# Kernel tuning notes

Measured on AMD Instinct MI355X. Metric: run time of the kernel, lower is better.

Reference implementation:

```python
import jax, jax.numpy as jnp
import numpy as np
from jax import lax

K = 3  # local kernel size (k in the module)
PAD = K // 2

def _conv2d(x, w, b, pad):
    # x: [B,Cin,H,W], w: [Cout,Cin,kh,kw]
    y = lax.conv_general_dilated(
        x, w, window_strides=(1, 1), padding=[(pad, pad), (pad, pad)],
        dimension_numbers=('NCHW', 'OIHW', 'NCHW'))
    return y + b[None, :, None, None]

def setup_inputs() -> dict:
    key = jax.random.key(0)
    ks = jax.random.split(key, 4)
    B, C, H, W = 8, 64, 256, 256
    lr_t = jax.random.normal(ks[0], (B, 3, H, W), dtype=jnp.float32)
    h_tm1 = jax.random.normal(ks[1], (B, C, H, W), dtype=jnp.float32)
    w1 = jax.random.normal(ks[2], (C, 3, 3, 3), dtype=jnp.float32) * (1.0 / np.sqrt(3 * 9))
    b1 = jnp.zeros((C,), dtype=jnp.float32)
    w2 = jax.random.normal(ks[3], (K * K, C, 1, 1), dtype=jnp.float32) * (1.0 / np.sqrt(C))
    b2 = jnp.zeros((K * K,), dtype=jnp.float32)
    return {"lr_t": lr_t, "h_tm1": h_tm1, "w1": w1, "b1": b1, "w2": w2, "b2": b2}

def reference(lr_t, h_tm1, w1, b1, w2, b2):
    B, C, H, W = h_tm1.shape
    # k_proj: Conv2d(3,dim,3,p=1) -> ReLU -> Conv2d(dim,k^2,1)
    kern = _conv2d(jax.nn.relu(_conv2d(lr_t, w1, b1, 1)), w2, b2, 0)  # [B,k^2,H,W]
    # Fused unfold * kernel -> sum over k^2 taps, without materializing [B,C,H,W,k^2].
    # F.unfold orders taps row-major: tap index = i*K + j.
    h_pad = jnp.pad(h_tm1, ((0, 0), (0, 0), (PAD, PAD), (PAD, PAD)))
    sim = jnp.zeros_like(h_tm1)
    for i in range(K):
        for j in range(K):
            shifted = lax.dynamic_slice(h_pad, (0, 0, i, j), (B, C, H, W))
            sim = sim + shifted * kern[:, i * K + j][:, None, :, :]
    return h_tm1 * jax.nn.sigmoid(sim)
```

## Files before the change

kernel.cpp:

```cpp
#include <hip/hip_runtime.h>
#include <hip/hip_bf16.h>
#include <math.h>

constexpr int B_  = 8;
constexpr int CIN = 3;
constexpr int C_  = 64;
constexpr int H_  = 256;
constexpr int W_  = 256;
constexpr int TAPS = 9;

typedef float f32x4 __attribute__((ext_vector_type(4)));

__global__ __launch_bounds__(256, 4)
void hsa_kern(const float* __restrict__ lr,
              const float* __restrict__ w1,
              const float* __restrict__ b1,
              const float* __restrict__ w2,
              const float* __restrict__ b2,
              float* __restrict__ kws)
{
    __shared__ float w2t[C_][12];

    const int tid = threadIdx.x;
    const int blk = blockIdx.x;
    const int b = blk / H_;
    const int y = blk % H_;

    for (int i = tid; i < TAPS * C_; i += 256) {
        const int t = i / C_;
        const int c = i % C_;
        w2t[c][t] = w2[i];
    }
    __syncthreads();

    const int x = tid;
    float win[CIN][3][3];
    #pragma unroll
    for (int ci = 0; ci < CIN; ++ci) {
        #pragma unroll
        for (int r = 0; r < 3; ++r) {
            const int yy = y + r - 1;
            const bool vy = (unsigned)yy < (unsigned)H_;
            const float* row = lr + ((size_t)(b * CIN + ci) * H_ + yy) * W_;
            win[ci][r][0] = (vy && x > 0)       ? row[x - 1] : 0.f;
            win[ci][r][1] = vy                   ? row[x]     : 0.f;
            win[ci][r][2] = (vy && x < W_ - 1)  ? row[x + 1] : 0.f;
        }
    }

    float acc[TAPS];
    #pragma unroll
    for (int t = 0; t < TAPS; ++t) acc[t] = b2[t];

    for (int c = 0; c < C_; ++c) {
        const float* wc = w1 + c * 27;
        float h0 = b1[c], h1 = 0.f, h2 = 0.f;
        #pragma unroll
        for (int r = 0; r < 3; ++r)
            #pragma unroll
            for (int j = 0; j < 3; ++j) {
                h0 = fmaf(wc[(0 * 3 + r) * 3 + j], win[0][r][j], h0);
                h1 = fmaf(wc[(1 * 3 + r) * 3 + j], win[1][r][j], h1);
                h2 = fmaf(wc[(2 * 3 + r) * 3 + j], win[2][r][j], h2);
            }
        const float hsum = fmaxf((h0 + h1) + h2, 0.f);

        const float4 wa = *(const float4*)&w2t[c][0];
        const float4 wb = *(const float4*)&w2t[c][4];
        const float  w8 = w2t[c][8];
        acc[0] = fmaf(wa.x, hsum, acc[0]);
        acc[1] = fmaf(wa.y, hsum, acc[1]);
        acc[2] = fmaf(wa.z, hsum, acc[2]);
        acc[3] = fmaf(wa.w, hsum, acc[3]);
        acc[4] = fmaf(wb.x, hsum, acc[4]);
        acc[5] = fmaf(wb.y, hsum, acc[5]);
        acc[6] = fmaf(wb.z, hsum, acc[6]);
        acc[7] = fmaf(wb.w, hsum, acc[7]);
        acc[8] = fmaf(w8,  hsum, acc[8]);
    }

    float* kr = kws + (size_t)(b * H_ + y) * TAPS * W_;
    #pragma unroll
    for (int t = 0; t < TAPS; ++t) kr[t * W_ + x] = acc[t];
}

__global__ __launch_bounds__(256, 8)
void hsa_gate(const float* __restrict__ hin,
              const float* __restrict__ kws,
              float* __restrict__ out)
{
    __shared__ float kernS[TAPS][W_];

    const int tid = threadIdx.x;
    const int bid = blockIdx.x;
    const int nb  = (bid & 7) * (B_ * H_ / 8) + (bid >> 3);
    const int b = nb / H_;
    const int y = nb % H_;

    const float* kr = kws + (size_t)(b * H_ + y) * TAPS * W_;
    for (int i = tid; i < TAPS * W_; i += 256)
        ((float*)kernS)[i] = kr[i];
    __syncthreads();

    const int lane = tid & 63;
    const int wav  = tid >> 6;
    const int x0   = lane * 4;

    float4 kt[TAPS];
    #pragma unroll
    for (int t = 0; t < TAPS; ++t) kt[t] = *(const float4*)&kernS[t][x0];

    #pragma unroll 4
    for (int cc = 0; cc < 16; ++cc) {
        const int c = wav * 16 + cc;
        const float* hb = hin + (size_t)(b * C_ + c) * H_ * W_;

        float4 rowv[3];
        float  lft[3], rgt[3];
        #pragma unroll
        for (int r = 0; r < 3; ++r) {
            const int yy = y + r - 1;
            const bool vy = (unsigned)yy < (unsigned)H_;
            float4 m;
            if (vy) m = *(const float4*)(hb + (size_t)yy * W_ + x0);
            else    m = make_float4(0.f, 0.f, 0.f, 0.f);
            rowv[r] = m;
            float l  = __shfl_up(m.w, 1);
            float rr = __shfl_down(m.x, 1);
            if (lane == 0)  l  = 0.f;
            if (lane == 63) rr = 0.f;
            lft[r] = l; rgt[r] = rr;
        }

        float sim0 = 0.f, sim1 = 0.f, sim2 = 0.f, sim3 = 0.f;
        #pragma unroll
        for (int r = 0; r < 3; ++r) {
            const float w6_0 = lft[r];
            const float w6_1 = rowv[r].x;
            const float w6_2 = rowv[r].y;
            const float w6_3 = rowv[r].z;
            const float w6_4 = rowv[r].w;
            const float w6_5 = rgt[r];
            {
                const float4 k4 = kt[r * 3 + 0];
                sim0 = fmaf(w6_0, k4.x, sim0);
                sim1 = fmaf(w6_1, k4.y, sim1);
                sim2 = fmaf(w6_2, k4.z, sim2);
                sim3 = fmaf(w6_3, k4.w, sim3);
            }
            {
                const float4 k4 = kt[r * 3 + 1];
                sim0 = fmaf(w6_1, k4.x, sim0);
                sim1 = fmaf(w6_2, k4.y, sim1);
                sim2 = fmaf(w6_3, k4.z, sim2);
                sim3 = fmaf(w6_4, k4.w, sim3);
            }
            {
                const float4 k4 = kt[r * 3 + 2];
                sim0 = fmaf(w6_2, k4.x, sim0);
                sim1 = fmaf(w6_3, k4.y, sim1);
                sim2 = fmaf(w6_4, k4.z, sim2);
                sim3 = fmaf(w6_5, k4.w, sim3);
            }
        }

        f32x4 o;
        o.x = rowv[1].x * __builtin_amdgcn_rcpf(1.f + __expf(-sim0));
        o.y = rowv[1].y * __builtin_amdgcn_rcpf(1.f + __expf(-sim1));
        o.z = rowv[1].z * __builtin_amdgcn_rcpf(1.f + __expf(-sim2));
        o.w = rowv[1].w * __builtin_amdgcn_rcpf(1.f + __expf(-sim3));
        __builtin_nontemporal_store(o, (f32x4*)(out + ((size_t)(b * C_ + c) * H_ + y) * W_ + x0));
    }
}

__global__ __launch_bounds__(256, 4)
void hsa_fused(const float* __restrict__ lr,
               const float* __restrict__ hin,
               const float* __restrict__ w1,
               const float* __restrict__ b1,
               const float* __restrict__ w2,
               const float* __restrict__ b2,
               float* __restrict__ out)
{
    __shared__ float kernS[TAPS][W_];
    __shared__ float w2t[C_][12];

    const int tid = threadIdx.x;
    const int blk = blockIdx.x;
    const int b = blk / H_;
    const int y = blk % H_;

    for (int i = tid; i < TAPS * C_; i += 256) {
        const int t = i / C_;
        const int c = i % C_;
        w2t[c][t] = w2[i];
    }
    __syncthreads();

    {
        const int x = tid;
        float win[CIN][3][3];
        #pragma unroll
        for (int ci = 0; ci < CIN; ++ci)
            #pragma unroll
            for (int r = 0; r < 3; ++r) {
                const int yy = y + r - 1;
                const bool vy = (unsigned)yy < (unsigned)H_;
                const float* row = lr + ((size_t)(b * CIN + ci) * H_ + yy) * W_;
                win[ci][r][0] = (vy && x > 0)      ? row[x - 1] : 0.f;
                win[ci][r][1] = vy                  ? row[x]     : 0.f;
                win[ci][r][2] = (vy && x < W_ - 1) ? row[x + 1] : 0.f;
            }

        float acc[TAPS];
        #pragma unroll
        for (int t = 0; t < TAPS; ++t) acc[t] = b2[t];

        for (int c = 0; c < C_; ++c) {
            const float* wc = w1 + c * 27;
            float h0 = b1[c], h1 = 0.f, h2 = 0.f;
            #pragma unroll
            for (int r = 0; r < 3; ++r)
                #pragma unroll
                for (int j = 0; j < 3; ++j) {
                    h0 = fmaf(wc[(0 * 3 + r) * 3 + j], win[0][r][j], h0);
                    h1 = fmaf(wc[(1 * 3 + r) * 3 + j], win[1][r][j], h1);
                    h2 = fmaf(wc[(2 * 3 + r) * 3 + j], win[2][r][j], h2);
                }
            const float hsum = fmaxf((h0 + h1) + h2, 0.f);
            const float4 wa = *(const float4*)&w2t[c][0];
            const float4 wb = *(const float4*)&w2t[c][4];
            const float  w8 = w2t[c][8];
            acc[0] = fmaf(wa.x, hsum, acc[0]);
            acc[1] = fmaf(wa.y, hsum, acc[1]);
            acc[2] = fmaf(wa.z, hsum, acc[2]);
            acc[3] = fmaf(wa.w, hsum, acc[3]);
            acc[4] = fmaf(wb.x, hsum, acc[4]);
            acc[5] = fmaf(wb.y, hsum, acc[5]);
            acc[6] = fmaf(wb.z, hsum, acc[6]);
            acc[7] = fmaf(wb.w, hsum, acc[7]);
            acc[8] = fmaf(w8,  hsum, acc[8]);
        }
        #pragma unroll
        for (int t = 0; t < TAPS; ++t) kernS[t][x] = acc[t];
    }
    __syncthreads();

    const int lane = tid & 63;
    const int wav  = tid >> 6;
    const int x0   = lane * 4;

    float4 kt[TAPS];
    #pragma unroll
    for (int t = 0; t < TAPS; ++t) kt[t] = *(const float4*)&kernS[t][x0];

    #pragma unroll 4
    for (int cc = 0; cc < 16; ++cc) {
        const int c = wav * 16 + cc;
        const float* hb = hin + (size_t)(b * C_ + c) * H_ * W_;

        float4 rowv[3];
        float  lft[3], rgt[3];
        #pragma unroll
        for (int r = 0; r < 3; ++r) {
            const int yy = y + r - 1;
            const bool vy = (unsigned)yy < (unsigned)H_;
            float4 m;
            if (vy) m = *(const float4*)(hb + (size_t)yy * W_ + x0);
            else    m = make_float4(0.f, 0.f, 0.f, 0.f);
            rowv[r] = m;
            float l  = __shfl_up(m.w, 1);
            float rr = __shfl_down(m.x, 1);
            if (lane == 0)  l  = 0.f;
            if (lane == 63) rr = 0.f;
            lft[r] = l; rgt[r] = rr;
        }

        float sim0 = 0.f, sim1 = 0.f, sim2 = 0.f, sim3 = 0.f;
        #pragma unroll
        for (int r = 0; r < 3; ++r) {
            const float w6_0 = lft[r];
            const float w6_1 = rowv[r].x;
            const float w6_2 = rowv[r].y;
            const float w6_3 = rowv[r].z;
            const float w6_4 = rowv[r].w;
            const float w6_5 = rgt[r];
            { const float4 k4 = kt[r*3+0];
              sim0 = fmaf(w6_0, k4.x, sim0); sim1 = fmaf(w6_1, k4.y, sim1);
              sim2 = fmaf(w6_2, k4.z, sim2); sim3 = fmaf(w6_3, k4.w, sim3); }
            { const float4 k4 = kt[r*3+1];
              sim0 = fmaf(w6_1, k4.x, sim0); sim1 = fmaf(w6_2, k4.y, sim1);
              sim2 = fmaf(w6_3, k4.z, sim2); sim3 = fmaf(w6_4, k4.w, sim3); }
            { const float4 k4 = kt[r*3+2];
              sim0 = fmaf(w6_2, k4.x, sim0); sim1 = fmaf(w6_3, k4.y, sim1);
              sim2 = fmaf(w6_4, k4.z, sim2); sim3 = fmaf(w6_5, k4.w, sim3); }
        }

        float4 o;
        o.x = rowv[1].x * __builtin_amdgcn_rcpf(1.f + __expf(-sim0));
        o.y = rowv[1].y * __builtin_amdgcn_rcpf(1.f + __expf(-sim1));
        o.z = rowv[1].z * __builtin_amdgcn_rcpf(1.f + __expf(-sim2));
        o.w = rowv[1].w * __builtin_amdgcn_rcpf(1.f + __expf(-sim3));
        *(float4*)(out + ((size_t)(b * C_ + c) * H_ + y) * W_ + x0) = o;
    }
}

extern "C" void kernel_launch(void* const* d_in, const int* in_sizes, int n_in,
                              void* d_out, int out_size, void* d_ws, size_t ws_size,
                              hipStream_t stream) {
    const float* lr  = (const float*)d_in[0];
    const float* hin = (const float*)d_in[1];
    const float* w1  = (const float*)d_in[2];
    const float* b1  = (const float*)d_in[3];
    const float* w2  = (const float*)d_in[4];
    const float* b2  = (const float*)d_in[5];
    float* out = (float*)d_out;

    const size_t kern_bytes = (size_t)B_ * H_ * TAPS * W_ * sizeof(float);

    if (ws_size >= kern_bytes) {
        float* kws = (float*)d_ws;
        hipLaunchKernelGGL(hsa_kern, dim3(B_ * H_), dim3(256), 0, stream,
                           lr, w1, b1, w2, b2, kws);
        hipLaunchKernelGGL(hsa_gate, dim3(B_ * H_), dim3(256), 0, stream,
                           hin, kws, out);
    } else {
        hipLaunchKernelGGL(hsa_fused, dim3(B_ * H_), dim3(256), 0, stream,
                           lr, hin, w1, b1, w2, b2, out);
    }
}
```

Baseline: 100.7 us.

## Restructure gate kernel into 8-row strips with rolling register window

The gate kernel now has each block handle an 8-row strip for 16 channels, instead of one row for all 64 channels. Each thread keeps a rolling 3-row window of input rows in registers, so every input row is loaded about once rather than three times. The per-row kernel weights are read straight from global memory instead of being staged through shared memory, which removes the barrier. Boundary handling moves to masks folded into the weights, and the nontemporal store becomes a plain store. In exchange, register pressure rises (launch bounds drop to 3 waves) and the grid shrinks to 1024 blocks, which may lower occupancy and latency hiding.

```diff
diff --git a/kernel.cpp b/kernel.cpp
--- a/kernel.cpp
+++ b/kernel.cpp
@@ -84,92 +84,106 @@
     for (int t = 0; t < TAPS; ++t) kr[t * W_ + x] = acc[t];
 }
 
-__global__ __launch_bounds__(256, 8)
+__global__ __launch_bounds__(256, 3)
 void hsa_gate(const float* __restrict__ hin,
               const float* __restrict__ kws,
               float* __restrict__ out)
 {
-    __shared__ float kernS[TAPS][W_];
-
     const int tid = threadIdx.x;
     const int bid = blockIdx.x;
-    const int nb  = (bid & 7) * (B_ * H_ / 8) + (bid >> 3);
-    const int b = nb / H_;
-    const int y = nb % H_;
-
-    const float* kr = kws + (size_t)(b * H_ + y) * TAPS * W_;
-    for (int i = tid; i < TAPS * W_; i += 256)
-        ((float*)kernS)[i] = kr[i];
-    __syncthreads();
+    const int nb  = (bid & 7) * 128 + (bid >> 3);
+    const int b     = nb >> 7;
+    const int strip = (nb >> 2) & 31;
+    const int cg    = nb & 3;
+    const int Y     = strip * 8;
 
     const int lane = tid & 63;
-    const int wav  = tid >> 6;
+    const int wv   = tid >> 6;
     const int x0   = lane * 4;
-
-    float4 kt[TAPS];
-    #pragma unroll
-    for (int t = 0; t < TAPS; ++t) kt[t] = *(const float4*)&kernS[t][x0];
-
-    #pragma unroll 4
-    for (int cc = 0; cc < 16; ++cc) {
-        const int c = wav * 16 + cc;
-        const float* hb = hin + (size_t)(b * C_ + c) * H_ * W_;
-
-        float4 rowv[3];
-        float  lft[3], rgt[3];
+    const int c0   = cg * 16 + wv * 4;
+
+    const size_t plane = (size_t)H_ * W_;
+    const float* hb = hin + ((size_t)b * C_ + c0) * plane;
+    float*       ob = out + ((size_t)b * C_ + c0) * plane;
+    const float* kb = kws + (size_t)b * H_ * (TAPS * W_);
+
+    const float lmask = (lane > 0)  ? 1.f : 0.f;
+    const float rmask = (lane < 63) ? 1.f : 0.f;
+
+    f32x4 win[3][4];
+    {
+        const int ym = (Y > 0) ? (Y - 1) : 0;
+        #pragma unroll
+        for (int i = 0; i < 4; ++i) {
+            win[0][i] = *(const f32x4*)(hb + i * plane + (size_t)ym      * W_ + x0);
+            win[1][i] = *(const f32x4*)(hb + i * plane + (size_t)Y       * W_ + x0);
+            win[2][i] = *(const f32x4*)(hb + i * plane + (size_t)(Y + 1) * W_ + x0);
+        }
+    }
+
+    #pragma unroll
+    for (int yy = 0; yy < 8; ++yy) {
+        const int yg = Y + yy;
+
+        const float* kr = kb + (size_t)yg * (TAPS * W_) + x0;
+        f32x4 kt[TAPS];
+        #pragma unroll
+        for (int t = 0; t < TAPS; ++t) kt[t] = *(const f32x4*)(kr + t * W_);
+
+        f32x4 nxt[4];
+        if (yy < 7) {
+            const int yn = (yg + 2 < H_) ? (yg + 2) : (H_ - 1);
+            #pragma unroll
+            for (int i = 0; i < 4; ++i)
+                nxt[i] = *(const f32x4*)(hb + i * plane + (size_t)yn * W_ + x0);
+        }
+
+        const float m0 = (yg > 0)      ? 1.f : 0.f;
+        const float m2 = (yg < H_ - 1) ? 1.f : 0.f;
+        #pragma unroll
+        for (int t = 0; t < 3; ++t) { kt[t] *= m0; kt[6 + t] *= m2; }
+        kt[0].x *= lmask; kt[3].x *= lmask; kt[6].x *= lmask;
+        kt[2].w *= rmask; kt[5].w *= rmask; kt[8].w *= rmask;
+
+        float sim[4][4];
+        #pragma unroll
+        for (int i = 0; i < 4; ++i)
+            #pragma unroll
+            for (int j = 0; j < 4; ++j) sim[i][j] = 0.f;
+
         #pragma unroll
         for (int r = 0; r < 3; ++r) {
-            const int yy = y + r - 1;
-            const bool vy = (unsigned)yy < (unsigned)H_;
-            float4 m;
-            if (vy) m = *(const float4*)(hb + (size_t)yy * W_ + x0);
-            else    m = make_float4(0.f, 0.f, 0.f, 0.f);
-            rowv[r] = m;
-            float l  = __shfl_up(m.w, 1);
-            float rr = __shfl_down(m.x, 1);
-            if (lane == 0)  l  = 0.f;
-            if (lane == 63) rr = 0.f;
-            lft[r] = l; rgt[r] = rr;
-        }
-
-        float sim0 = 0.f, sim1 = 0.f, sim2 = 0.f, sim3 = 0.f;
-        #pragma unroll
-        for (int r = 0; r < 3; ++r) {
-            const float w6_0 = lft[r];
-            const float w6_1 = rowv[r].x;
-            const float w6_2 = rowv[r].y;
-            const float w6_3 = rowv[r].z;
-            const float w6_4 = rowv[r].w;
-            const float w6_5 = rgt[r];
-            {
-                const float4 k4 = kt[r * 3 + 0];
-                sim0 = fmaf(w6_0, k4.x, sim0);
-                sim1 = fmaf(w6_1, k4.y, sim1);
-                sim2 = fmaf(w6_2, k4.z, sim2);
-                sim3 = fmaf(w6_3, k4.w, sim3);
+            const int sl = (yy + r) % 3;
+            const f32x4 k0 = kt[r * 3 + 0];
+            const f32x4 k1 = kt[r * 3 + 1];
+            const f32x4 k2 = kt[r * 3 + 2];
+            #pragma unroll
+            for (int i = 0; i < 4; ++i) {
+                const f32x4 cv = win[sl][i];
+                const float l  = __shfl_up(cv.w, 1);
+                const float rr = __shfl_down(cv.x, 1);
+                sim[i][0] = fmaf(l,    k0.x, fmaf(cv.x, k1.x, fmaf(cv.y, k2.x, sim[i][0])));
+                sim[i][1] = fmaf(cv.x, k0.y, fmaf(cv.y, k1.y, fmaf(cv.z, k2.y, sim[i][1])));
+                sim[i][2] = fmaf(cv.y, k0.z, fmaf(cv.z, k1.z, fmaf(cv.w, k2.z, sim[i][2])));
+                sim[i][3] = fmaf(cv.z, k0.w, fmaf(cv.w, k1.w, fmaf(rr,   k2.w, sim[i][3])));
             }
-            {
-                const float4 k4 = kt[r * 3 + 1];
-                sim0 = fmaf(w6_1, k4.x, sim0);
-                sim1 = fmaf(w6_2, k4.y, sim1);
-                sim2 = fmaf(w6_3, k4.z, sim2);
-                sim3 = fmaf(w6_4, k4.w, sim3);
-            }
-            {
-                const float4 k4 = kt[r * 3 + 2];
-                sim0 = fmaf(w6_2, k4.x, sim0);
-                sim1 = fmaf(w6_3, k4.y, sim1);
-                sim2 = fmaf(w6_4, k4.z, sim2);
-                sim3 = fmaf(w6_5, k4.w, sim3);
-            }
-        }
-
-        f32x4 o;
-        o.x = rowv[1].x * __builtin_amdgcn_rcpf(1.f + __expf(-sim0));
-        o.y = rowv[1].y * __builtin_amdgcn_rcpf(1.f + __expf(-sim1));
-        o.z = rowv[1].z * __builtin_amdgcn_rcpf(1.f + __expf(-sim2));
-        o.w = rowv[1].w * __builtin_amdgcn_rcpf(1.f + __expf(-sim3));
-        __builtin_nontemporal_store(o, (f32x4*)(out + ((size_t)(b * C_ + c) * H_ + y) * W_ + x0));
+        }
+
+        #pragma unroll
+        for (int i = 0; i < 4; ++i) {
+            const f32x4 ctr = win[(yy + 1) % 3][i];
+            f32x4 o;
+            o.x = ctr.x * __builtin_amdgcn_rcpf(1.f + __expf(-sim[i][0]));
+            o.y = ctr.y * __builtin_amdgcn_rcpf(1.f + __expf(-sim[i][1]));
+            o.z = ctr.z * __builtin_amdgcn_rcpf(1.f + __expf(-sim[i][2]));
+            o.w = ctr.w * __builtin_amdgcn_rcpf(1.f + __expf(-sim[i][3]));
+            *(f32x4*)(ob + i * plane + (size_t)yg * W_ + x0) = o;
+        }
+
+        if (yy < 7) {
+            #pragma unroll
+            for (int i = 0; i < 4; ++i) win[yy % 3][i] = nxt[i];
+        }
     }
 }
 
@@ -322,7 +336,7 @@
         float* kws = (float*)d_ws;
         hipLaunchKernelGGL(hsa_kern, dim3(B_ * H_), dim3(256), 0, stream,
                            lr, w1, b1, w2, b2, kws);
-        hipLaunchKernelGGL(hsa_gate, dim3(B_ * H_), dim3(256), 0, stream,
+        hipLaunchKernelGGL(hsa_gate, dim3(1024), dim3(256), 0, stream,
                            hin, kws, out);
     } else {
         hipLaunchKernelGGL(hsa_fused, dim3(B_ * H_), dim3(256), 0, stream,
```

New measurement: 105.1 us. +4.5%, slower.
